# Kernel tuning notes

Hardware: AMD Instinct MI355X
Metric: run time of the kernel (lower is better)

## Reference

```python
import jax, jax.numpy as jnp
import numpy as np

B, S, D, H = 4, 2048, 1024, 16
HD = D // H  # head dim = 64


def setup_inputs() -> dict:
    key = jax.random.key(0)
    ks = jax.random.split(key, 10)
    std = 1.0 / np.sqrt(D)
    return {
        "Q": jax.random.normal(ks[0], (B, S, D), jnp.float32),
        "Q_lev": jax.random.normal(ks[1], (B, S, D), jnp.float32),
        "K": jax.random.normal(ks[2], (B, S, D), jnp.float32),
        "K_lev": jax.random.normal(ks[3], (B, S, D), jnp.float32),
        "V": jax.random.normal(ks[4], (B, S, D), jnp.float32),
        "V_lev": jax.random.normal(ks[5], (B, S, D), jnp.float32),
        "Wq": jax.random.normal(ks[6], (D, D), jnp.float32) * std,
        "bq": jnp.zeros((D,), jnp.float32),
        "Wk": jax.random.normal(ks[7], (D, D), jnp.float32) * std,
        "bk": jnp.zeros((D,), jnp.float32),
        "Wv": jax.random.normal(ks[8], (D, D), jnp.float32) * std,
        "bv": jnp.zeros((D,), jnp.float32),
        "Wo": jax.random.normal(ks[9], (D, D), jnp.float32) * std,
        "bo": jnp.zeros((D,), jnp.float32),
    }


def _heads(x):
    # [B,S,D] -> [B,H,S,HD]
    return x.reshape(B, S, H, HD).transpose(0, 2, 1, 3)


def reference(Q, Q_lev, K, K_lev, V, V_lev, Wq, bq, Wk, bk, Wv, bv, Wo, bo):
    q = _heads(Q @ Wq + bq + Q_lev)
    k = _heads(K @ Wk + bk + K_lev)
    v = _heads(V @ Wv + bv + V_lev)
    scores = jnp.einsum("bhqd,bhkd->bhqk", q, k) / np.sqrt(HD).astype(np.float32)
    probs = jax.nn.softmax(scores, axis=-1)  # attn_dropout rate 0 -> identity
    ctx = jnp.einsum("bhqk,bhkd->bhqd", probs, v)
    ctx = ctx.transpose(0, 2, 1, 3).reshape(B, S, D)
    return ctx @ Wo + bo  # proj_dropout rate 0 -> identity
```

## Files before the change

kernel.cpp:

```cpp
#include <hip/hip_runtime.h>
#include <hip/hip_bf16.h>

#define Bq 4
#define Sq 2048
#define Dq 1024
#define Hq 16
#define HDq 64
#define MR (Bq*Sq)

typedef __attribute__((ext_vector_type(8))) short bf16x8;
typedef __attribute__((ext_vector_type(4))) float f32x4;
typedef __attribute__((ext_vector_type(16))) float f32x16;

__device__ __forceinline__ unsigned short f2bf(float f){
  unsigned int x = __builtin_bit_cast(unsigned int, f);
  x += 0x7fffu + ((x >> 16) & 1u);
  return (unsigned short)(x >> 16);
}

__device__ __forceinline__ unsigned cvtpk(float a, float b){
  unsigned r;
  asm("v_cvt_pk_bf16_f32 %0, %1, %2" : "=v"(r) : "v"(a), "v"(b));
  return r;
}

#define MFMA(a,b,c)   __builtin_amdgcn_mfma_f32_16x16x32_bf16((a),(b),(c),0,0,0)
#define MFMA32(a,b,c) __builtin_amdgcn_mfma_f32_32x32x16_bf16((a),(b),(c),0,0,0)

#define SC_Q 0.18033688f

__device__ __forceinline__ void gload16(const unsigned short* g, unsigned short* l){
  __builtin_amdgcn_global_load_lds(
      (const __attribute__((address_space(1))) void*)g,
      (__attribute__((address_space(3))) void*)l, 16, 0, 0);
}

__global__ __launch_bounds__(256) void cvt_bf16x3(
    const float* __restrict__ X0, const float* __restrict__ X1, const float* __restrict__ X2,
    unsigned short* __restrict__ O0, unsigned short* __restrict__ O1, unsigned short* __restrict__ O2)
{
  const int z = blockIdx.y;
  const float* X = z==0?X0 : z==1?X1 : X2;
  unsigned short* O = z==0?O0 : z==1?O1 : O2;
  const size_t i = ((size_t)blockIdx.x*256 + threadIdx.x)*8;
  const float4 a = *(const float4*)(X+i);
  const float4 b = *(const float4*)(X+i+4);
  union { unsigned u[4]; int4 v; } pk;
  pk.u[0] = cvtpk(a.x, a.y);
  pk.u[1] = cvtpk(a.z, a.w);
  pk.u[2] = cvtpk(b.x, b.y);
  pk.u[3] = cvtpk(b.z, b.w);
  *(int4*)(O+i) = pk.v;
}

__global__ __launch_bounds__(256) void transpose_w(
    const float* __restrict__ W0, const float* __restrict__ W1,
    const float* __restrict__ W2, const float* __restrict__ W3,
    unsigned short* __restrict__ T0, unsigned short* __restrict__ T1,
    unsigned short* __restrict__ T2, unsigned short* __restrict__ T3)
{
  __shared__ float tile[32][33];
  const int z = blockIdx.z;
  const float* W = z==0?W0 : z==1?W1 : z==2?W2 : W3;
  unsigned short* T = z==0?T0 : z==1?T1 : z==2?T2 : T3;
  const int k0 = blockIdx.x*32, n0 = blockIdx.y*32;
  const int tx = threadIdx.x & 31, ty = threadIdx.x >> 5;
  #pragma unroll
  for (int i=0;i<4;i++) tile[ty+i*8][tx] = W[(size_t)(k0+ty+i*8)*Dq + n0+tx];
  __syncthreads();
  #pragma unroll
  for (int i=0;i<4;i++) T[(size_t)(n0+ty+i*8)*Dq + k0+tx] = f2bf(tile[tx][ty+i*8]);
}

__global__ __launch_bounds__(256) void transpose_v(
    const unsigned short* __restrict__ Vb, unsigned short* __restrict__ Vo)
{
  __shared__ unsigned short t2[64][72];
  const int bh = blockIdx.y;
  const int b = bh >> 4, h = bh & 15;
  const int s0 = blockIdx.x * 64;
  const int tid = threadIdx.x;
  const int r = tid >> 3, c8 = tid & 7;
  #pragma unroll
  for (int i=0;i<2;i++){
    int s = r + i*32;
    union { int4 v; unsigned short u[8]; } uu;
    uu.v = *(const int4*)(Vb + ((size_t)b*Sq + s0 + s)*Dq + h*HDq + c8*8);
    #pragma unroll
    for (int jj=0;jj<8;jj++){
      int j = (jj + c8) & 7;
      t2[c8*8 + j][s] = uu.u[j];
    }
  }
  __syncthreads();
  #pragma unroll
  for (int i=0;i<2;i++){
    int d = r + i*32;
    *(int4*)(Vo + ((size_t)bh*HDq + d)*Sq + s0 + c8*8) = *(const int4*)&t2[d][c8*8];
  }
}

__device__ __forceinline__ void gemm_loop(const unsigned short* __restrict__ A,
    const unsigned short* __restrict__ Bt,
    int bm, int bn, unsigned short* Al, unsigned short* Bl, f32x4 acc[4][4])
{
  const int tid = threadIdx.x;
  const int lane = tid & 63, wid = tid >> 6;
  const int lr = lane & 15, lg = lane >> 4;
  const int wm = wid >> 1, wn = wid & 1;

  const int srow = wid*32 + (lane >> 3), sch = (lane & 7)*8;
  const unsigned short* As = A  + (size_t)(bm*128 + srow)*Dq + sch;
  const unsigned short* Bs = Bt + (size_t)(bn*128 + srow)*Dq + sch;

  #define STAGE(buf, k0) { \
    unsigned short* Ald = Al + (buf)*8192 + wid*2048; \
    unsigned short* Bld = Bl + (buf)*8192 + wid*2048; \
    _Pragma("unroll") \
    for (int i=0;i<4;i++){ \
      gload16(As + (size_t)i*8*Dq + (k0), Ald + i*512); \
      gload16(Bs + (size_t)i*8*Dq + (k0), Bld + i*512); \
    } }

  STAGE(0, 0);
  __syncthreads();
  int cur = 0;
  for (int k0 = 0; k0 < Dq; k0 += 64) {
    if (k0 + 64 < Dq) STAGE(cur^1, k0+64);
    const unsigned short* Ac = Al + cur*8192;
    const unsigned short* Bc = Bl + cur*8192;
    #pragma unroll
    for (int kc=0;kc<2;kc++){
      bf16x8 af[4], bfr[4];
      #pragma unroll
      for (int mt=0;mt<4;mt++) af[mt]  = *(const bf16x8*)(Ac + (wm*64+mt*16+lr)*64 + kc*32 + lg*8);
      #pragma unroll
      for (int nt=0;nt<4;nt++) bfr[nt] = *(const bf16x8*)(Bc + (wn*64+nt*16+lr)*64 + kc*32 + lg*8);
      #pragma unroll
      for (int mt=0;mt<4;mt++)
        #pragma unroll
        for (int nt=0;nt<4;nt++)
          acc[mt][nt] = MFMA(af[mt], bfr[nt], acc[mt][nt]);
    }
    asm volatile("s_waitcnt vmcnt(0)" ::: "memory");
    __syncthreads();
    cur ^= 1;
  }
  #undef STAGE
}

__global__ __launch_bounds__(256) void proj_gemm(
    const unsigned short* __restrict__ Aq, const unsigned short* __restrict__ Ak, const unsigned short* __restrict__ Av,
    const float* __restrict__ Lq, const float* __restrict__ Lk, const float* __restrict__ Lv,
    const unsigned short* __restrict__ Tq, const unsigned short* __restrict__ Tk, const unsigned short* __restrict__ Tv,
    const float* __restrict__ bqp, const float* __restrict__ bkp, const float* __restrict__ bvp,
    unsigned short* __restrict__ Oq, unsigned short* __restrict__ Ok, unsigned short* __restrict__ Ov)
{
  __shared__ __align__(16) unsigned short Al[2*128*64];
  __shared__ __align__(16) unsigned short Bl[2*128*64];

  const int bid = blockIdx.x;
  const int swz = (bid & 7)*192 + (bid >> 3);
  const int z   = swz >> 9;
  const int rem = swz & 511;
  const int bm  = rem >> 3, bn = rem & 7;

  const unsigned short* A = z==0?Aq : z==1?Ak : Av;
  const float* Lev = z==0?Lq : z==1?Lk : Lv;
  const unsigned short* Bt = z==0?Tq : z==1?Tk : Tv;
  const float* bias = z==0?bqp : z==1?bkp : bvp;
  unsigned short* Out = z==0?Oq : z==1?Ok : Ov;
  const float scl = (z==0) ? SC_Q : 1.0f;

  f32x4 acc[4][4];
  #pragma unroll
  for (int mt=0;mt<4;mt++)
    #pragma unroll
    for (int nt=0;nt<4;nt++) acc[mt][nt] = (f32x4){0.f,0.f,0.f,0.f};

  gemm_loop(A, Bt, bm, bn, Al, Bl, acc);

  const int tid = threadIdx.x, lane = tid&63, wid = tid>>6;
  const int lr = lane&15, lg = lane>>4, wm = wid>>1, wn = wid&1;
  const int colb = bn*128 + wn*64;
  float bcol[4];
  #pragma unroll
  for (int nt=0;nt<4;nt++) bcol[nt] = bias[colb + nt*16 + lr];
  #pragma unroll
  for (int mt=0;mt<4;mt++){
    int g = bm*128 + wm*64 + mt*16 + lg*4;
    #pragma unroll
    for (int r=0;r<4;r++){
      size_t ro = (size_t)(g+r)*Dq;
      #pragma unroll
      for (int nt=0;nt<4;nt++){
        int col = colb + nt*16 + lr;
        float v = (acc[mt][nt][r] + bcol[nt] + Lev[ro + col]) * scl;
        Out[ro + col] = f2bf(v);
      }
    }
  }
}

__device__ __forceinline__ float comb_max(float x){ return fmaxf(x, __shfl_xor(x, 32, 64)); }
__device__ __forceinline__ float comb_sum(float x){ return x + __shfl_xor(x, 32, 64); }

__device__ __forceinline__ void pack_p(const f32x16& t, int hi, bf16x8& c0, bf16x8& c1){
  unsigned w[8];
  #pragma unroll
  for (int j=0;j<8;j++) w[j] = cvtpk(t[2*j], t[2*j+1]);
  unsigned x[8];
  #pragma unroll
  for (int j=0;j<8;j++) x[j] = (unsigned)__shfl_xor((int)w[j], 32, 64);
  union { unsigned u[4]; bf16x8 v; } p0, p1;
  p0.u[0] = hi ? x[2] : w[0];
  p0.u[1] = hi ? x[3] : w[1];
  p0.u[2] = hi ? w[2] : x[0];
  p0.u[3] = hi ? w[3] : x[1];
  p1.u[0] = hi ? x[6] : w[4];
  p1.u[1] = hi ? x[7] : w[5];
  p1.u[2] = hi ? w[6] : x[4];
  p1.u[3] = hi ? w[7] : x[5];
  c0 = p0.v; c1 = p1.v;
}

__global__ __launch_bounds__(512, 4) void attn_k(
    const unsigned short* qb, const unsigned short* __restrict__ kb,
    const unsigned short* __restrict__ vt, unsigned short* cb)
{
  __shared__ unsigned short Kl[2][64*64];
  __shared__ unsigned short Vl[2][64*64];
  __shared__ float Rl[8][32];

  const int bid = blockIdx.x;
  const int swz = (bid & 7)*64 + (bid >> 3);
  const int qt = swz & 7, bh = swz >> 3;
  const int b = bh >> 4, h = bh & 15;
  const size_t base = (size_t)b*Sq*Dq + (size_t)h*HDq;

  const int tid = threadIdx.x, lane = tid & 63, wid = tid >> 6;
  const int ln31 = lane & 31, hi = lane >> 5;
  const int q0 = qt*256 + wid*32;

  bf16x8 qf[4];
  {
    const unsigned short* qp = qb + base + (size_t)(q0 + ln31)*Dq + hi*8;
    #pragma unroll
    for (int dk=0;dk<4;dk++) qf[dk] = *(const bf16x8*)(qp + dk*16);
  }

  const int kRow = tid >> 3, kCh = tid & 7;
  const unsigned short* kSrc = kb + base + (size_t)kRow*Dq + kCh*8;
  const unsigned short* vSrc = vt + ((size_t)bh*HDq + kRow)*Sq + kCh*8;
  const int wOff = kRow*64 + ((kCh ^ (kRow & 7))*8);

  int4 kreg = *(const int4*)kSrc;
  int4 vreg = *(const int4*)vSrc;
  *(int4*)&Kl[0][wOff] = kreg;
  *(int4*)&Vl[0][wOff] = vreg;

  f32x16 o0 = (f32x16)(0.0f), o1 = (f32x16)(0.0f);
  float m = -1e30f, l = 0.f;

  for (int kt = 0; kt < Sq/64; ++kt){
    __syncthreads();
    const int p = kt & 1;
    if (kt+1 < Sq/64){
      kreg = *(const int4*)(kSrc + (size_t)(kt+1)*64*Dq);
      vreg = *(const int4*)(vSrc + (kt+1)*64);
    }

    f32x16 t0 = (f32x16)(0.0f), t1 = (f32x16)(0.0f);
    __builtin_amdgcn_s_setprio(1);
    #pragma unroll
    for (int dk=0;dk<4;dk++){
      const int c = hi + dk*2;
      bf16x8 kf0 = *(const bf16x8*)&Kl[p][(ln31)*64    + ((c ^ (ln31 & 7))*8)];
      bf16x8 kf1 = *(const bf16x8*)&Kl[p][(32+ln31)*64 + ((c ^ (ln31 & 7))*8)];
      t0 = MFMA32(kf0, qf[dk], t0);
      t1 = MFMA32(kf1, qf[dk], t1);
    }
    __builtin_amdgcn_s_setprio(0);

    float tmax = t0[0];
    #pragma unroll
    for (int r=1;r<16;r++) tmax = fmaxf(tmax, t0[r]);
    #pragma unroll
    for (int r=0;r<16;r++) tmax = fmaxf(tmax, t1[r]);
    tmax = comb_max(tmax);
    if (__any(tmax > m + 8.0f)){
      float mn = fmaxf(m, tmax);
      float al = __builtin_amdgcn_exp2f(m - mn);
      m = mn;
      l *= al;
      if (hi == 0) Rl[wid][ln31] = al;
      asm volatile("" ::: "memory");
      f32x4 av[4];
      #pragma unroll
      for (int g=0; g<4; g++) av[g] = *(const f32x4*)&Rl[wid][g*8 + hi*4];
      #pragma unroll
      for (int r=0;r<16;r++){ o0[r] *= av[r>>2][r&3]; o1[r] *= av[r>>2][r&3]; }
    }
    float tsum = 0.f;
    #pragma unroll
    for (int r=0;r<16;r++){
      float a0 = __builtin_amdgcn_exp2f(t0[r] - m); t0[r] = a0; tsum += a0;
      float a1 = __builtin_amdgcn_exp2f(t1[r] - m); t1[r] = a1; tsum += a1;
    }
    l += comb_sum(tsum);

    bf16x8 pa0, pa1, pa2, pa3;
    pack_p(t0, hi, pa0, pa1);
    pack_p(t1, hi, pa2, pa3);
    __builtin_amdgcn_s_setprio(1);
    #pragma unroll
    for (int c=0;c<4;c++){
      bf16x8 pa = c==0?pa0 : c==1?pa1 : c==2?pa2 : pa3;
      const int vc = 2*c + hi;
      bf16x8 vf0 = *(const bf16x8*)&Vl[p][(ln31)*64    + ((vc ^ (ln31 & 7))*8)];
      bf16x8 vf1 = *(const bf16x8*)&Vl[p][(32+ln31)*64 + ((vc ^ (ln31 & 7))*8)];
      o0 = MFMA32(pa, vf0, o0);
      o1 = MFMA32(pa, vf1, o1);
    }
    __builtin_amdgcn_s_setprio(0);

    if (kt+1 < Sq/64){
      const int pn = p ^ 1;
      *(int4*)&Kl[pn][wOff] = kreg;
      *(int4*)&Vl[pn][wOff] = vreg;
    }
  }

  float linv = __builtin_amdgcn_rcpf(l);
  if (hi == 0) Rl[wid][ln31] = linv;
  asm volatile("" ::: "memory");
  f32x4 lv[4];
  #pragma unroll
  for (int g=0; g<4; g++) lv[g] = *(const f32x4*)&Rl[wid][g*8 + hi*4];
  #pragma unroll
  for (int r=0;r<16;r++){
    int q = (r&3) + 8*(r>>2) + 4*hi;
    size_t ro = base + (size_t)(q0 + q)*Dq;
    cb[ro + ln31]      = f2bf(o0[r] * lv[r>>2][r&3]);
    cb[ro + 32 + ln31] = f2bf(o1[r] * lv[r>>2][r&3]);
  }
}

__global__ __launch_bounds__(256) void out_gemm(
    const unsigned short* __restrict__ Ctx, const unsigned short* __restrict__ To,
    const float* __restrict__ bop, float* __restrict__ Out)
{
  __shared__ __align__(16) unsigned short Al[2*128*64];
  __shared__ __align__(16) unsigned short Bl[2*128*64];

  const int bid = blockIdx.x;
  const int swz = (bid & 7)*64 + (bid >> 3);
  const int bm  = swz >> 3, bn = swz & 7;

  f32x4 acc[4][4];
  #pragma unroll
  for (int mt=0;mt<4;mt++)
    #pragma unroll
    for (int nt=0;nt<4;nt++) acc[mt][nt] = (f32x4){0.f,0.f,0.f,0.f};

  gemm_loop(Ctx, To, bm, bn, Al, Bl, acc);

  const int tid = threadIdx.x, lane = tid&63, wid = tid>>6;
  const int lr = lane&15, lg = lane>>4, wm = wid>>1, wn = wid&1;
  const int colb = bn*128 + wn*64;
  float bcol[4];
  #pragma unroll
  for (int nt=0;nt<4;nt++) bcol[nt] = bop[colb + nt*16 + lr];
  #pragma unroll
  for (int mt=0;mt<4;mt++){
    int g = bm*128 + wm*64 + mt*16 + lg*4;
    #pragma unroll
    for (int r=0;r<4;r++){
      size_t ro = (size_t)(g+r)*Dq;
      #pragma unroll
      for (int nt=0;nt<4;nt++){
        int col = colb + nt*16 + lr;
        Out[ro + col] = acc[mt][nt][r] + bcol[nt];
      }
    }
  }
}

extern "C" void kernel_launch(void* const* d_in, const int* in_sizes, int n_in,
                              void* d_out, int out_size, void* d_ws, size_t ws_size,
                              hipStream_t stream) {
  const float* Q    = (const float*)d_in[0];
  const float* Qlev = (const float*)d_in[1];
  const float* K    = (const float*)d_in[2];
  const float* Klev = (const float*)d_in[3];
  const float* V    = (const float*)d_in[4];
  const float* Vlev = (const float*)d_in[5];
  const float* Wq   = (const float*)d_in[6];
  const float* bq   = (const float*)d_in[7];
  const float* Wk   = (const float*)d_in[8];
  const float* bk   = (const float*)d_in[9];
  const float* Wv   = (const float*)d_in[10];
  const float* bv   = (const float*)d_in[11];
  const float* Wo   = (const float*)d_in[12];
  const float* bo   = (const float*)d_in[13];

  unsigned short* qbuf = (unsigned short*)d_ws;
  unsigned short* kbuf = qbuf + (size_t)MR*Dq;
  unsigned short* vbuf = kbuf + (size_t)MR*Dq;
  unsigned short* xq   = vbuf + (size_t)MR*Dq;
  unsigned short* xk   = xq   + (size_t)MR*Dq;
  unsigned short* xv   = xk   + (size_t)MR*Dq;
  unsigned short* Tq   = xv   + (size_t)MR*Dq;
  unsigned short* Tk   = Tq + (size_t)Dq*Dq;
  unsigned short* Tv   = Tk + (size_t)Dq*Dq;
  unsigned short* To   = Tv + (size_t)Dq*Dq;
  unsigned short* vtb  = xq;

  cvt_bf16x3<<<dim3(MR*Dq/(256*8), 3), 256, 0, stream>>>(Q, K, V, xq, xk, xv);
  transpose_w<<<dim3(Dq/32, Dq/32, 4), 256, 0, stream>>>(Wq,Wk,Wv,Wo, Tq,Tk,Tv,To);
  proj_gemm<<<dim3(1536), 256, 0, stream>>>(
      xq,xk,xv, Qlev,Klev,Vlev, Tq,Tk,Tv, bq,bk,bv, qbuf,kbuf,vbuf);
  transpose_v<<<dim3(Sq/64, Bq*Hq), 256, 0, stream>>>(vbuf, vtb);
  attn_k<<<dim3(512), 512, 0, stream>>>(qbuf, kbuf, vtb, qbuf);
  out_gemm<<<dim3(512), 256, 0, stream>>>(qbuf, To, bo, (float*)d_out);
}
```

Measured before the change: 261.6 us.

## Triple-buffer GEMM K-loop with BK=32, swizzled LDS and partial waits

Restructures the shared GEMM main loop used by the projection and output kernels. It moves from double-buffered 64-wide K tiles to triple-buffered 32-wide tiles with XOR-swizzled LDS columns to avoid bank conflicts, and waits on only the older loads via vmcnt(4) so prefetch overlaps compute. It also raises MFMA priority with s_setprio and sets launch bounds to 3 blocks per CU, helped by the smaller LDS footprint. In exchange there are twice as many barriers per K, and the extra in-flight loads add register pressure.

```diff
diff --git a/kernel.cpp b/kernel.cpp
--- a/kernel.cpp
+++ b/kernel.cpp
@@ -109,55 +109,62 @@
   const int lr = lane & 15, lg = lane >> 4;
   const int wm = wid >> 1, wn = wid & 1;
 
-  const int srow = wid*32 + (lane >> 3), sch = (lane & 7)*8;
-  const unsigned short* As = A  + (size_t)(bm*128 + srow)*Dq + sch;
-  const unsigned short* Bs = Bt + (size_t)(bn*128 + srow)*Dq + sch;
-
-  #define STAGE(buf, k0) { \
-    unsigned short* Ald = Al + (buf)*8192 + wid*2048; \
-    unsigned short* Bld = Bl + (buf)*8192 + wid*2048; \
+  #define STG(buf, k0) { \
+    unsigned short* Ad = Al + (buf)*4096 + wid*512; \
+    unsigned short* Bd = Bl + (buf)*4096 + wid*512; \
     _Pragma("unroll") \
-    for (int i=0;i<4;i++){ \
-      gload16(As + (size_t)i*8*Dq + (k0), Ald + i*512); \
-      gload16(Bs + (size_t)i*8*Dq + (k0), Bld + i*512); \
+    for (int i=0;i<2;i++){ \
+      const int row = i*64 + (tid>>2); \
+      const int cl  = (tid&3) ^ ((row>>1)&3); \
+      gload16(A  + (size_t)(bm*128+row)*Dq + (k0) + cl*8, Ad + i*2048); \
+      gload16(Bt + (size_t)(bn*128+row)*Dq + (k0) + cl*8, Bd + i*2048); \
     } }
 
-  STAGE(0, 0);
+  STG(0, 0);
+  STG(1, 32);
+  asm volatile("s_waitcnt vmcnt(4)" ::: "memory");
   __syncthreads();
-  int cur = 0;
-  for (int k0 = 0; k0 < Dq; k0 += 64) {
-    if (k0 + 64 < Dq) STAGE(cur^1, k0+64);
-    const unsigned short* Ac = Al + cur*8192;
-    const unsigned short* Bc = Bl + cur*8192;
-    #pragma unroll
-    for (int kc=0;kc<2;kc++){
-      bf16x8 af[4], bfr[4];
+
+  const int cr = (lg ^ ((lr >> 1) & 3)) * 8;
+  for (int t = 0; t < 32; ++t){
+    const int buf = t % 3;
+    const unsigned short* Ab = Al + buf*4096;
+    const unsigned short* Bb = Bl + buf*4096;
+    bf16x8 af[4], bfv[4];
+    #pragma unroll
+    for (int mt=0;mt<4;mt++) af[mt]  = *(const bf16x8*)(Ab + (wm*64+mt*16+lr)*32 + cr);
+    #pragma unroll
+    for (int nt=0;nt<4;nt++) bfv[nt] = *(const bf16x8*)(Bb + (wn*64+nt*16+lr)*32 + cr);
+
+    if (t + 2 < 32) {
+      STG((t+2)%3, (t+2)*32);
+      asm volatile("s_waitcnt vmcnt(4)" ::: "memory");
+    } else if (t == 30) {
+      asm volatile("s_waitcnt vmcnt(0)" ::: "memory");
+    }
+
+    __builtin_amdgcn_s_setprio(1);
+    #pragma unroll
+    for (int mt=0;mt<4;mt++)
       #pragma unroll
-      for (int mt=0;mt<4;mt++) af[mt]  = *(const bf16x8*)(Ac + (wm*64+mt*16+lr)*64 + kc*32 + lg*8);
-      #pragma unroll
-      for (int nt=0;nt<4;nt++) bfr[nt] = *(const bf16x8*)(Bc + (wn*64+nt*16+lr)*64 + kc*32 + lg*8);
-      #pragma unroll
-      for (int mt=0;mt<4;mt++)
-        #pragma unroll
-        for (int nt=0;nt<4;nt++)
-          acc[mt][nt] = MFMA(af[mt], bfr[nt], acc[mt][nt]);
-    }
-    asm volatile("s_waitcnt vmcnt(0)" ::: "memory");
+      for (int nt=0;nt<4;nt++)
+        acc[mt][nt] = MFMA(af[mt], bfv[nt], acc[mt][nt]);
+    __builtin_amdgcn_s_setprio(0);
+
     __syncthreads();
-    cur ^= 1;
-  }
-  #undef STAGE
-}
-
-__global__ __launch_bounds__(256) void proj_gemm(
+  }
+  #undef STG
+}
+
+__global__ __launch_bounds__(256, 3) void proj_gemm(
     const unsigned short* __restrict__ Aq, const unsigned short* __restrict__ Ak, const unsigned short* __restrict__ Av,
     const float* __restrict__ Lq, const float* __restrict__ Lk, const float* __restrict__ Lv,
     const unsigned short* __restrict__ Tq, const unsigned short* __restrict__ Tk, const unsigned short* __restrict__ Tv,
     const float* __restrict__ bqp, const float* __restrict__ bkp, const float* __restrict__ bvp,
     unsigned short* __restrict__ Oq, unsigned short* __restrict__ Ok, unsigned short* __restrict__ Ov)
 {
-  __shared__ __align__(16) unsigned short Al[2*128*64];
-  __shared__ __align__(16) unsigned short Bl[2*128*64];
+  __shared__ __align__(16) unsigned short Al[3*4096];
+  __shared__ __align__(16) unsigned short Bl[3*4096];
 
   const int bid = blockIdx.x;
   const int swz = (bid & 7)*192 + (bid >> 3);
@@ -346,12 +353,12 @@
   }
 }
 
-__global__ __launch_bounds__(256) void out_gemm(
+__global__ __launch_bounds__(256, 3) void out_gemm(
     const unsigned short* __restrict__ Ctx, const unsigned short* __restrict__ To,
     const float* __restrict__ bop, float* __restrict__ Out)
 {
-  __shared__ __align__(16) unsigned short Al[2*128*64];
-  __shared__ __align__(16) unsigned short Bl[2*128*64];
+  __shared__ __align__(16) unsigned short Al[3*4096];
+  __shared__ __align__(16) unsigned short Bl[3*4096];
 
   const int bid = blockIdx.x;
   const int swz = (bid & 7)*64 + (bid >> 3);
```

Result: no change. 258.9 us (-1.0%).
